# Kernel tuning notes

Measured on AMD Instinct MI355X. Metric: run time of the kernel, lower is better.

## Reference

```python
import jax, jax.numpy as jnp
import numpy as np
import math

N, E, D, H = 50000, 1600000, 128, 8
DH = D // H  # per-head dim
EPS = 1e-5   # batchnorm eps


def _attn(q_in, k_in, v_in, Wq, Wk, Wv, src, dst):
    # GAT-style edge attention: score = exp(clip(<K[src],Q[dst]>/sqrt(DH), -5, 5))
    Q = (q_in @ Wq.T).reshape(-1, H, DH)
    K = (k_in @ Wk.T).reshape(-1, H, DH)
    V = (v_in @ Wv.T).reshape(-1, H, DH)
    score = jnp.exp(jnp.clip((K[src] * Q[dst]).sum(-1) / math.sqrt(DH), -5.0, 5.0))  # [E,H]
    wV = jax.ops.segment_sum(V[src] * score[:, :, None], dst, num_segments=N)  # [N,H,DH]
    z = jax.ops.segment_sum(score, dst, num_segments=N)                         # [N,H]
    return (wV / z[:, :, None]).reshape(-1, D)


def _bn(x, gamma, beta):
    # BatchNorm1d in training mode: biased batch stats over nodes
    m = x.mean(0)
    v = x.var(0)
    return (x - m) / jnp.sqrt(v + EPS) * gamma + beta


def setup_inputs() -> dict:
    key = jax.random.key(0)
    ks = iter(jax.random.split(key, 48))

    def w(shape, scale=None):
        s = scale if scale is not None else 1.0 / math.sqrt(shape[-1])
        return jax.random.normal(next(ks), shape, jnp.float32) * s

    inp = dict(
        h=w((N, D), 1.0),
        sv=w((N, D), 1.0),
        src=jax.random.randint(next(ks), (E,), 0, N, jnp.int32),
        dst=jax.random.randint(next(ks), (E,), 0, N, jnp.int32),
    )
    for nm in ["Wq_sv", "Wk_sv", "Wv_sv", "Wq_cv", "Wk_cv", "Wv_cv",
               "Wq_sh", "Wk_sh", "Wv_sh"]:
        inp[nm] = w((D, D))
    inp.update(
        Wo=w((D, 2 * D)), bo=jnp.zeros((D,), jnp.float32),
        Wo_h=w((D, 2 * D)), bo_h=jnp.zeros((D,), jnp.float32),
        W1=w((2 * D, D)), b1=jnp.zeros((2 * D,), jnp.float32),
        W2=w((D, 2 * D)), b2=jnp.zeros((D,), jnp.float32),
        W1h=w((2 * D, D)), b1h=jnp.zeros((2 * D,), jnp.float32),
        W2h=w((D, 2 * D)), b2h=jnp.zeros((D,), jnp.float32),
        Wg1=w((D, D)), bg1=jnp.zeros((D,), jnp.float32),
        Wg2=w((D, D)), bg2=jnp.zeros((D,), jnp.float32),
        gbn1=jnp.ones((D,), jnp.float32), bbn1=jnp.zeros((D,), jnp.float32),
        gbn2=jnp.ones((D,), jnp.float32), bbn2=jnp.zeros((D,), jnp.float32),
        gbn1h=jnp.ones((D,), jnp.float32), bbn1h=jnp.zeros((D,), jnp.float32),
        gbn2h=jnp.ones((D,), jnp.float32), bbn2h=jnp.zeros((D,), jnp.float32),
    )
    return inp


def reference(h, sv, src, dst,
              Wq_sv, Wk_sv, Wv_sv, Wq_cv, Wk_cv, Wv_cv, Wq_sh, Wk_sh, Wv_sh,
              Wo, bo, Wo_h, bo_h,
              W1, b1, W2, b2, W1h, b1h, W2h, b2h,
              Wg1, bg1, Wg2, bg2,
              gbn1, bbn1, gbn2, bbn2, gbn1h, bbn1h, gbn2h, bbn2h):
    h_in1, sv_in1 = h, sv
    # --- h branch ---
    a_self = _attn(h, h, h, Wq_sv, Wk_sv, Wv_sv, src, dst)
    a_cross = _attn(h, sv, sv, Wq_cv, Wk_cv, Wv_cv, src, dst)
    hO = jnp.concatenate([a_self, a_cross], -1) @ Wo.T + bo
    h1 = _bn(h_in1 + hO, gbn1, bbn1)
    ffn = jax.nn.relu(h1 @ W1.T + b1) @ W2.T + b2
    h_out = _bn(h1 + ffn, gbn2, bbn2)
    # --- state-vector branch ---
    a_self_h = _attn(sv, sv, sv, Wq_sh, Wk_sh, Wv_sh, src, dst)
    # faithful to source: cross_attention_v weights reused here
    a_cross_h = _attn(sv, h_in1, h_in1, Wq_cv, Wk_cv, Wv_cv, src, dst)
    svO = jnp.concatenate([a_self_h, a_cross_h], -1) @ Wo_h.T + bo_h
    g1 = jax.nn.sigmoid(h_in1 @ Wg1.T + bg1)
    sv1 = _bn((1.0 - g1) * sv_in1 + g1 * svO, gbn1h, bbn1h)
    ffn_h = jax.nn.relu(sv1 @ W1h.T + b1h) @ W2h.T + b2h
    g2 = jax.nn.sigmoid(h_in1 @ Wg2.T + bg2)
    sv_out = _bn((1.0 - g2) * sv1 + g2 * ffn_h, gbn2h, bbn2h)
    return (h_out, sv_out)
```

## Files before the change

kernel.cpp:

```cpp
#include <hip/hip_runtime.h>

typedef _Float16 f16x8 __attribute__((ext_vector_type(8)));
typedef _Float16 f16x2 __attribute__((ext_vector_type(2)));
typedef __fp16 fp16x2_raw __attribute__((ext_vector_type(2)));
typedef float f32x4 __attribute__((ext_vector_type(4)));
typedef float f32x2 __attribute__((ext_vector_type(2)));
typedef unsigned int uint32;
typedef unsigned short ushort16;
typedef unsigned char uchar;

#define EPS_BN 1e-5f

__device__ __forceinline__ uint32 pk16(float a, float b){
  fp16x2_raw h = __builtin_amdgcn_cvt_pkrtz(a, b);
  return *(uint32*)&h;
}
__device__ __forceinline__ ushort16 f2h(float f){
  _Float16 h = (_Float16)f;
  union { _Float16 h; ushort16 u; } c; c.h = h; return c.u;
}
__device__ __forceinline__ uchar f2fp8(float f){
  uint32 p = __builtin_amdgcn_cvt_pk_fp8_f32(f, f, 0, false);
  return (uchar)(p & 0xff);
}
__device__ __forceinline__ f32x2 fp8pair_lo(uint32 w){
  return __builtin_amdgcn_cvt_pk_f32_fp8(w, false);
}
__device__ __forceinline__ f32x2 fp8pair_hi(uint32 w){
  return __builtin_amdgcn_cvt_pk_f32_fp8(w, true);
}

struct WEnt { const float* s; const float* s2; ushort16* d; int KD, MD, nfrag; };
struct WConv { WEnt e[16]; };

__global__ __launch_bounds__(256) void conv_w_k(WConv a){
  WEnt t = a.e[blockIdx.y];
  int fid = blockIdx.x * 256 + threadIdx.x;
  if (fid >= t.nfrag) return;
  int lane = fid & 63, sm = fid >> 6;
  int MT = t.MD >> 4;
  int s = sm / MT, m = sm - s * MT;
  int row = m * 16 + (lane & 15);
  int col = s * 32 + (lane >> 4) * 8;
  const float* sp = t.s;
  if (t.s2 && row >= 128){ sp = t.s2; row -= 128; }
  const float* p = sp + (size_t)row * t.KD + col;
  uint4 o;
  o.x = pk16(p[0], p[1]); o.y = pk16(p[2], p[3]);
  o.z = pk16(p[4], p[5]); o.w = pk16(p[6], p[7]);
  *(uint4*)(t.d + (size_t)fid * 8) = o;
}

__global__ __launch_bounds__(256) void conv2_k(const float* __restrict__ a, const float* __restrict__ b,
                                               ushort16* __restrict__ da, ushort16* __restrict__ db, int n){
  const float* s = blockIdx.y ? b : a;
  ushort16* d = blockIdx.y ? db : da;
  int i = (blockIdx.x * 256 + threadIdx.x) * 4;
  if (i >= n) return;
  float4 v = *(const float4*)(s + i);
  uint2 p;
  p.x = pk16(v.x, v.y);
  p.y = pk16(v.z, v.w);
  *(uint2*)(d + i) = p;
}

__global__ void hist_k(const int* __restrict__ dst, int* __restrict__ cnt, int E){
  int i = blockIdx.x * blockDim.x + threadIdx.x;
  int stride = gridDim.x * blockDim.x;
  for (; i < E; i += stride) atomicAdd(&cnt[dst[i]], 1);
}

__global__ __launch_bounds__(256) void scan_part_k(const int* __restrict__ cnt, int* __restrict__ bsum, int N){
  int tid = threadIdx.x, lane = tid & 63, wv = tid >> 6;
  int base = blockIdx.x * 1024 + tid * 4;
  int ts = 0;
  #pragma unroll
  for (int j = 0; j < 4; j++) if (base + j < N) ts += cnt[base + j];
  #pragma unroll
  for (int d = 1; d < 64; d <<= 1) ts += __shfl_xor(ts, d);
  __shared__ int wt[4];
  if (lane == 0) wt[wv] = ts;
  __syncthreads();
  if (tid == 0) bsum[blockIdx.x] = wt[0] + wt[1] + wt[2] + wt[3];
}

__global__ __launch_bounds__(64) void scan_top_k(int* __restrict__ bsum, int nb){
  int tid = threadIdx.x;
  int v = (tid < nb) ? bsum[tid] : 0;
  int inc = v;
  #pragma unroll
  for (int d = 1; d < 64; d <<= 1){
    int t = __shfl_up(inc, d);
    if (tid >= d) inc += t;
  }
  if (tid < nb) bsum[tid] = inc - v;
}

__global__ __launch_bounds__(256) void scan_out_k(const int* __restrict__ cnt, const int* __restrict__ bsum,
                                                  int* __restrict__ row_off, int* __restrict__ cursor,
                                                  int* __restrict__ bcur,
                                                  int N, int E, int shift){
  int tid = threadIdx.x, lane = tid & 63, wv = tid >> 6;
  int base = blockIdx.x * 1024 + tid * 4;
  int c[4]; int ts = 0;
  #pragma unroll
  for (int j = 0; j < 4; j++){ c[j] = (base + j < N) ? cnt[base + j] : 0; ts += c[j]; }
  int inc = ts;
  #pragma unroll
  for (int d = 1; d < 64; d <<= 1){
    int t = __shfl_up(inc, d);
    if (lane >= d) inc += t;
  }
  int wexcl = inc - ts;
  __shared__ int wt[4];
  if (lane == 63) wt[wv] = inc;
  __syncthreads();
  int woff = 0;
  for (int w = 0; w < 4; w++) if (w < wv) woff += wt[w];
  int off = bsum[blockIdx.x] + woff + wexcl;
  int mask = (1 << shift) - 1;
  #pragma unroll
  for (int j = 0; j < 4; j++){
    int d = base + j;
    if (d < N){
      row_off[d] = off; cursor[d] = off;
      if ((d & mask) == 0) bcur[d >> shift] = off;
      off += c[j];
    }
  }
  if (blockIdx.x == 0 && tid == 0) row_off[N] = E;
}

#define BIN_TB 512
#define BIN_TILE 4096
__global__ __launch_bounds__(512) void bin_k(const int* __restrict__ src, const int* __restrict__ dst,
                                             int* __restrict__ bcur, uint2* __restrict__ ebuf,
                                             int E, int shift, int B){
  __shared__ int lhist[128];
  __shared__ int lstart[128];
  __shared__ int gbase[128];
  __shared__ uint2 lpair[BIN_TILE];
  int tid = threadIdx.x;
  int base = blockIdx.x * BIN_TILE;
  int cnt = E - base; if (cnt > BIN_TILE) cnt = BIN_TILE;
  if (tid < 128) lhist[tid] = 0;
  __syncthreads();
  int myb[8], myrank[8];
  uint2 myp[8];
  int nmine = 0;
  #pragma unroll
  for (int j = 0; j < 8; j++){
    int i = tid + j * BIN_TB;
    if (i < cnt){
      int s = src[base + i], d = dst[base + i];
      int b = d >> shift;
      myp[nmine] = make_uint2((uint32)s, (uint32)d);
      myb[nmine] = b;
      myrank[nmine] = atomicAdd(&lhist[b], 1);
      nmine++;
    }
  }
  __syncthreads();
  if (tid == 0){
    int run = 0;
    for (int b = 0; b < B; b++){ lstart[b] = run; run += lhist[b]; }
  }
  __syncthreads();
  if (tid < B) gbase[tid] = atomicAdd(&bcur[tid], lhist[tid]);
  for (int j = 0; j < nmine; j++){
    lpair[lstart[myb[j]] + myrank[j]] = myp[j];
  }
  __syncthreads();
  for (int i = tid; i < cnt; i += BIN_TB){
    uint2 p = lpair[i];
    int b = (int)(p.y >> shift);
    ebuf[gbase[b] + (i - lstart[b])] = p;
  }
}

__global__ __launch_bounds__(512) void bfill_k(const uint2* __restrict__ ebuf, const int* __restrict__ row_off,
                                               int* __restrict__ cursor, int* __restrict__ esrc,
                                               int shift, int N){
  int b = blockIdx.x;
  int d0 = b << shift;
  int d1 = (b + 1) << shift; if (d1 > N) d1 = N;
  if (d0 >= N) return;
  int e0 = row_off[d0], e1 = row_off[d1];
  for (int i = e0 + (int)threadIdx.x; i < e1; i += 512){
    uint2 p = ebuf[i];
    int pos = atomicAdd(&cursor[p.y], 1);
    esrc[pos] = (int)p.x;
  }
}

__global__ __launch_bounds__(256) void gemm_qkv_k(
    const ushort16* __restrict__ Xq, const ushort16* __restrict__ Xkv,
    const ushort16* __restrict__ Wq, const ushort16* __restrict__ Wk, const ushort16* __restrict__ Wv,
    ushort16* __restrict__ Qo, uchar* __restrict__ KV8, int N)
{
  __shared__ _Float16 Qs[4][16 * 136];
  __shared__ uchar Ks[4][16 * 136];
  __shared__ uchar Vs[4][16 * 136];
  int lane = threadIdx.x & 63, wv = threadIdx.x >> 6;
  int l15 = lane & 15, kq = lane >> 4;
  int rowbase = (blockIdx.x * 4 + wv) * 16;
  int row = rowbase + l15;
  int rc = row < N ? row : N - 1;
  const f16x8* aq = (const f16x8*)(Xq + (size_t)rc * 128 + kq * 8);
  const f16x8* ak = (const f16x8*)(Xkv + (size_t)rc * 128 + kq * 8);
  f16x8 Aq[4], Ak[4];
  #pragma unroll
  for (int s = 0; s < 4; s++){ Aq[s] = aq[s * 4]; Ak[s] = ak[s * 4]; }
  const f16x8* Wqf = (const f16x8*)Wq;
  const f16x8* Wkf = (const f16x8*)Wk;
  const f16x8* Wvf = (const f16x8*)Wv;
  f32x4 q[8], k[8], v[8];
  #pragma unroll
  for (int m = 0; m < 8; m++){ q[m] = (f32x4)(0.f); k[m] = (f32x4)(0.f); v[m] = (f32x4)(0.f); }
  #pragma unroll
  for (int s = 0; s < 4; s++){
    #pragma unroll
    for (int m = 0; m < 8; m++){
      int fi = (s * 8 + m) * 64 + lane;
      q[m] = __builtin_amdgcn_mfma_f32_16x16x32_f16(Aq[s], Wqf[fi], q[m], 0, 0, 0);
      k[m] = __builtin_amdgcn_mfma_f32_16x16x32_f16(Ak[s], Wkf[fi], k[m], 0, 0, 0);
      v[m] = __builtin_amdgcn_mfma_f32_16x16x32_f16(Ak[s], Wvf[fi], v[m], 0, 0, 0);
    }
  }
  #pragma unroll
  for (int m = 0; m < 8; m++){
    int col = m * 16 + l15;
    #pragma unroll
    for (int r = 0; r < 4; r++){
      int lrow = kq * 4 + r;
      Qs[wv][lrow * 136 + col] = (_Float16)q[m][r];
      Ks[wv][lrow * 136 + col] = f2fp8(k[m][r]);
      Vs[wv][lrow * 136 + col] = f2fp8(v[m][r]);
    }
  }
  #pragma unroll
  for (int p = 0; p < 4; p++){
    int lrow = p * 4 + (lane >> 4);
    int rr = rowbase + lrow;
    int col8 = l15 * 8;
    if (rr < N){
      uint4 qv = *(uint4*)&Qs[wv][lrow * 136 + col8];
      *(uint4*)(Qo + (size_t)rr * 128 + col8) = qv;
      uint2 kv = *(uint2*)&Ks[wv][lrow * 136 + col8];
      *(uint2*)(KV8 + (size_t)rr * 256 + col8) = kv;
      uint2 vv = *(uint2*)&Vs[wv][lrow * 136 + col8];
      *(uint2*)(KV8 + (size_t)rr * 256 + 128 + col8) = vv;
    }
  }
}

template<int KD, int MD, int EPI, int ABN, int ST, int GS>
__global__ __launch_bounds__(256) void gemm_k(
    const ushort16* __restrict__ X, const ushort16* __restrict__ W,
    const float* __restrict__ bias, const float* __restrict__ bias2,
    const ushort16* __restrict__ resb, const ushort16* __restrict__ gatep,
    const float* __restrict__ rstats, const float* __restrict__ rg, const float* __restrict__ rb,
    const float* __restrict__ astats, const float* __restrict__ ag, const float* __restrict__ ab,
    ushort16* __restrict__ outb, float* __restrict__ stats_out, int N, float invN)
{
  constexpr int KS = KD / 32;
  constexpr int MT = MD / 16;
  constexpr int LSTR = MD + 8;
  __shared__ _Float16 Os[4][16 * LSTR];
  int lane = threadIdx.x & 63, wv = threadIdx.x >> 6;
  int l15 = lane & 15, kq = lane >> 4;
  int rowbase = (blockIdx.x * 4 + wv) * 16;
  int row = rowbase + l15;
  int rc = row < N ? row : N - 1;
  const f16x8* ap = (const f16x8*)(X + (size_t)rc * KD + kq * 8);
  f16x8 a[KS];
  #pragma unroll
  for (int s = 0; s < KS; s++) a[s] = ap[s * 4];
  if constexpr (ABN){
    #pragma unroll
    for (int s = 0; s < KS; s++){
      #pragma unroll
      for (int j = 0; j < 8; j++){
        int c = s * 32 + kq * 8 + j;
        float mm = astats[c] * invN;
        float var = astats[128 + c] * invN - mm * mm;
        float rs = rsqrtf(var + EPS_BN);
        float scc = rs * ag[c];
        float shh = ab[c] - mm * scc;
        a[s][j] = (_Float16)((float)a[s][j] * scc + shh);
      }
    }
  }
  const f16x8* Wf = (const f16x8*)W;
  f32x4 acc[MT];
  #pragma unroll
  for (int m = 0; m < MT; m++) acc[m] = (f32x4)(0.f);
  #pragma unroll
  for (int s = 0; s < KS; s++){
    #pragma unroll
    for (int m = 0; m < MT; m++){
      acc[m] = __builtin_amdgcn_mfma_f32_16x16x32_f16(a[s], Wf[(s * MT + m) * 64 + lane], acc[m], 0, 0, 0);
    }
  }
  float ps[MT], ps2[MT];
  if constexpr (ST){
    #pragma unroll
    for (int m = 0; m < MT; m++){ ps[m] = 0.f; ps2[m] = 0.f; }
  }
  int r0 = rowbase + kq * 4;
  #pragma unroll
  for (int m = 0; m < MT; m++){
    int col = m * 16 + l15;
    float bv;
    if (bias2 && col >= 128) bv = bias2[col - 128];
    else bv = bias[col];
    float sc = 0.f, sh = 0.f;
    if constexpr (EPI == 5 || EPI == 6){
      float mm = rstats[col] * invN;
      float var = rstats[128 + col] * invN - mm * mm;
      float rs = rsqrtf(var + EPS_BN);
      sc = rs * rg[col]; sh = rb[col] - mm * sc;
    }
    #pragma unroll
    for (int r = 0; r < 4; r++){
      int rr = r0 + r;
      float v;
      {
        int rrc = rr < N ? rr : N - 1;
        v = acc[m][r] + bv;
        if constexpr (EPI == 1) v = fmaxf(v, 0.f);
        if constexpr (EPI == 2) v = 1.f / (1.f + __expf(-v));
        if constexpr (EPI == 3){
          union { ushort16 u; _Float16 h; } cv; cv.u = resb[(size_t)rrc * 128 + col];
          v += (float)cv.h;
        }
        if constexpr (EPI == 5){
          union { ushort16 u; _Float16 h; } cv; cv.u = resb[(size_t)rrc * 128 + col];
          v += (float)cv.h * sc + sh;
        }
        if constexpr (EPI == 4 || EPI == 6){
          union { ushort16 u; _Float16 h; } gv; gv.u = gatep[(size_t)rrc * GS + col];
          union { ushort16 u; _Float16 h; } cv; cv.u = resb[(size_t)rrc * 128 + col];
          float g = (float)gv.h;
          float rv = (float)cv.h;
          if constexpr (EPI == 6) rv = rv * sc + sh;
          v = (1.f - g) * rv + g * v;
        }
      }
      Os[wv][(kq * 4 + r) * LSTR + col] = (_Float16)v;
      if constexpr (ST){
        if (rr < N){ ps[m] += v; ps2[m] += v * v; }
      }
    }
  }
  if constexpr (MD == 128){
    #pragma unroll
    for (int p = 0; p < 4; p++){
      int lrow = p * 4 + (lane >> 4);
      int rr = rowbase + lrow;
      int col8 = l15 * 8;
      if (rr < N){
        uint4 ov = *(uint4*)&Os[wv][lrow * LSTR + col8];
        *(uint4*)(outb + (size_t)rr * MD + col8) = ov;
      }
    }
  } else {
    #pragma unroll
    for (int p = 0; p < 8; p++){
      int lrow = p * 2 + (lane >> 5);
      int rr = rowbase + lrow;
      int col8 = (lane & 31) * 8;
      if (rr < N){
        uint4 ov = *(uint4*)&Os[wv][lrow * LSTR + col8];
        *(uint4*)(outb + (size_t)rr * MD + col8) = ov;
      }
    }
  }
  if constexpr (ST){
    __shared__ float sst[4][128];
    __shared__ float sst2[4][128];
    #pragma unroll
    for (int m = 0; m < MT; m++){
      float s = ps[m], s2 = ps2[m];
      s  += __shfl_xor(s, 16);  s  += __shfl_xor(s, 32);
      s2 += __shfl_xor(s2, 16); s2 += __shfl_xor(s2, 32);
      if (lane < 16){ sst[wv][m * 16 + l15] = s; sst2[wv][m * 16 + l15] = s2; }
    }
    __syncthreads();
    int tid = threadIdx.x;
    if (tid < 128){
      atomicAdd(&stats_out[tid], sst[0][tid] + sst[1][tid] + sst[2][tid] + sst[3][tid]);
    } else {
      int c = tid - 128;
      atomicAdd(&stats_out[tid], sst2[0][c] + sst2[1][c] + sst2[2][c] + sst2[3][c]);
    }
  }
}

__global__ __launch_bounds__(256) void attn4_k(
    const ushort16* __restrict__ Qa, const ushort16* __restrict__ Qb,
    const ushort16* __restrict__ Qc, const ushort16* __restrict__ Qd,
    const uchar* __restrict__ KVa, const uchar* __restrict__ KVb,
    const uchar* __restrict__ KVc, const uchar* __restrict__ KVd,
    const int* __restrict__ row_off, const int* __restrict__ esrc,
    ushort16* __restrict__ cat_h, ushort16* __restrict__ cat_sv, int N)
{
  int wv = threadIdx.x >> 6, lane = threadIdx.x & 63;
  int n = blockIdx.x * 4 + wv;
  if (n >= N) return;
  int h = lane >> 5, j = lane & 31;
  uint32 j4 = (uint32)j * 4u;
  const float QS = 0.25f * 1.44269504088896f;
  const float CL = 7.21347520444482f;
  const ushort16* Qp[4] = {Qa, Qb, Qc, Qd};
  const uchar* KVp[4] = {KVa, KVb, KVc, KVd};
  f32x2 q01[4], q23[4];
  #pragma unroll
  for (int t = 0; t < 4; t++){
    uint2 u = *(const uint2*)(Qp[t] + (size_t)n * 128 + j4);
    f16x2 t0 = *(f16x2*)&u.x, t1 = *(f16x2*)&u.y;
    q01[t].x = (float)t0.x * QS; q01[t].y = (float)t0.y * QS;
    q23[t].x = (float)t1.x * QS; q23[t].y = (float)t1.y * QS;
  }
  int e0 = row_off[n], e1 = row_off[n + 1];
  int itmax = (e1 - e0 + 1) >> 1;
  f32x2 ac01[4], ac23[4];
  #pragma unroll
  for (int t = 0; t < 4; t++){ ac01[t] = (f32x2)(0.f); ac23[t] = (f32x2)(0.f); }
  f32x2 z01 = (f32x2)(0.f), z23 = (f32x2)(0.f);
  int e = e0 + h;
  int s = (e < e1) ? esrc[e] : -1;
  uint32 off = ((uint32)(s < 0 ? 0 : s) << 8) + j4;
  uint32 kc_[4], vc_[4];
  #pragma unroll
  for (int t = 0; t < 4; t++){
    kc_[t] = *(const uint32*)(KVp[t] + off);
    vc_[t] = *(const uint32*)(KVp[t] + off + 128);
  }
  for (int it = 0; it < itmax; ++it){
    int e2 = e + 2;
    int s2 = (e2 < e1) ? esrc[e2] : -1;
    uint32 off2 = ((uint32)(s2 < 0 ? 0 : s2) << 8) + j4;
    uint32 kn_[4], vn_[4];
    #pragma unroll
    for (int t = 0; t < 4; t++){
      kn_[t] = *(const uint32*)(KVp[t] + off2);
      vn_[t] = *(const uint32*)(KVp[t] + off2 + 128);
    }
    if (s >= 0){
      float d[4];
      #pragma unroll
      for (int t = 0; t < 4; t++){
        f32x2 k01 = fp8pair_lo(kc_[t]), k23 = fp8pair_hi(kc_[t]);
        f32x2 dd = k01 * q01[t] + k23 * q23[t];
        d[t] = dd.x + dd.y;
      }
      #pragma unroll
      for (int t = 0; t < 4; t++){
        d[t] += __shfl_xor(d[t], 1);
        d[t] += __shfl_xor(d[t], 2);
      }
      float sc4[4];
      #pragma unroll
      for (int t = 0; t < 4; t++)
        sc4[t] = __builtin_amdgcn_exp2f(__builtin_amdgcn_fmed3f(d[t], -CL, CL));
      #pragma unroll
      for (int t = 0; t < 4; t++){
        f32x2 v01 = fp8pair_lo(vc_[t]), v23 = fp8pair_hi(vc_[t]);
        f32x2 sv; sv.x = sc4[t]; sv.y = sc4[t];
        ac01[t] += sv * v01;
        ac23[t] += sv * v23;
      }
      z01.x += sc4[0]; z01.y += sc4[1];
      z23.x += sc4[2]; z23.y += sc4[3];
    }
    e = e2; s = s2;
    #pragma unroll
    for (int t = 0; t < 4; t++){ kc_[t] = kn_[t]; vc_[t] = vn_[t]; }
  }
  #pragma unroll
  for (int t = 0; t < 4; t++){
    f32x2 x;
    x.x = __shfl_xor(ac01[t].x, 32); x.y = __shfl_xor(ac01[t].y, 32); ac01[t] += x;
    x.x = __shfl_xor(ac23[t].x, 32); x.y = __shfl_xor(ac23[t].y, 32); ac23[t] += x;
  }
  {
    f32x2 x;
    x.x = __shfl_xor(z01.x, 32); x.y = __shfl_xor(z01.y, 32); z01 += x;
    x.x = __shfl_xor(z23.x, 32); x.y = __shfl_xor(z23.y, 32); z23 += x;
  }
  size_t nbh = (size_t)n * 256 + j4;
  uint2 o;
  if (h == 0){
    float rz = __builtin_amdgcn_rcpf(z01.x);
    o.x = pk16(ac01[0].x * rz, ac01[0].y * rz);
    o.y = pk16(ac23[0].x * rz, ac23[0].y * rz);
    *(uint2*)(cat_h + nbh) = o;
    rz = __builtin_amdgcn_rcpf(z23.x);
    o.x = pk16(ac01[2].x * rz, ac01[2].y * rz);
    o.y = pk16(ac23[2].x * rz, ac23[2].y * rz);
    *(uint2*)(cat_sv + nbh) = o;
  } else {
    float rz = __builtin_amdgcn_rcpf(z01.y);
    o.x = pk16(ac01[1].x * rz, ac01[1].y * rz);
    o.y = pk16(ac23[1].x * rz, ac23[1].y * rz);
    *(uint2*)(cat_h + nbh + 128) = o;
    rz = __builtin_amdgcn_rcpf(z23.y);
    o.x = pk16(ac01[3].x * rz, ac01[3].y * rz);
    o.y = pk16(ac23[3].x * rz, ac23[3].y * rz);
    *(uint2*)(cat_sv + nbh + 128) = o;
  }
}

__global__ __launch_bounds__(256) void bn_apply_k(
    const ushort16* __restrict__ x, const float* __restrict__ stats,
    const float* __restrict__ gamma, const float* __restrict__ beta,
    float* __restrict__ outf, int total4, float invN)
{
  int i = blockIdx.x * 256 + threadIdx.x;
  if (i >= total4) return;
  uint2 xp = *(const uint2*)(x + (size_t)i * 4);
  f16x2 x01 = *(f16x2*)&xp.x, x23 = *(f16x2*)&xp.y;
  float xv[4] = {(float)x01.x, (float)x01.y, (float)x23.x, (float)x23.y};
  int c0 = (i * 4) & 127;
  float o[4];
  #pragma unroll
  for (int j = 0; j < 4; j++){
    int c = c0 + j;
    float m = stats[c] * invN;
    float var = stats[128 + c] * invN - m * m;
    float rstd = rsqrtf(var + EPS_BN);
    o[j] = (xv[j] - m) * rstd * gamma[c] + beta[c];
  }
  *(float4*)(outf + (size_t)i * 4) = make_float4(o[0], o[1], o[2], o[3]);
}

extern "C" void kernel_launch(void* const* d_in, const int* in_sizes, int n_in,
                              void* d_out, int out_size, void* d_ws, size_t ws_size,
                              hipStream_t stream) {
  const float* h   = (const float*)d_in[0];
  const float* sv  = (const float*)d_in[1];
  const int* src   = (const int*)d_in[2];
  const int* dst   = (const int*)d_in[3];
  const int N = in_sizes[0] / 128;
  const int E = in_sizes[2];

  char* wsb = (char*)d_ws;
  size_t o = 0;
  auto take = [&](size_t bytes)->size_t{
    size_t r = o;
    o = (o + bytes + 255) & ~(size_t)255;
    return r;
  };
  size_t ebuf_bytes = (size_t)E * 8;
  if (ebuf_bytes < (size_t)N * 256) ebuf_bytes = (size_t)N * 256;
  size_t cnt_off    = take((size_t)N * 4);
  size_t stats_off  = take(4 * 256 * 4);
  size_t rowoff_off = take((size_t)(N + 1) * 4);
  size_t cursor_off = take((size_t)N * 4);
  size_t bsum_off   = take(256 * 4);
  size_t bcur_off   = take(128 * 4);
  size_t esrc_off   = take((size_t)E * 4);
  size_t ebuf_off   = take(ebuf_bytes);
  size_t wpool_off  = take((size_t)376832 * 2);
  size_t hf_off     = take((size_t)N * 128 * 2);
  size_t svf_off    = take((size_t)N * 128 * 2);
  size_t cath_off   = take((size_t)N * 256 * 2);
  size_t catsv_off  = take((size_t)N * 256 * 2);
  size_t K81_off    = take((size_t)N * 128);
  size_t V81_off    = take((size_t)N * 128);
  size_t K82_off    = take((size_t)N * 128);
  size_t V82_off    = take((size_t)N * 128);
  size_t Q1_off     = take((size_t)N * 128 * 2);
  size_t Q2_off     = take((size_t)N * 128 * 2);
  size_t X1_off     = take((size_t)N * 128 * 2);
  size_t X2_off     = take((size_t)N * 128 * 2);
  size_t G_off      = take((size_t)N * 256 * 2);

  int*    cnt     = (int*)(wsb + cnt_off);
  float*  stats   = (float*)(wsb + stats_off);
  int*    row_off = (int*)(wsb + rowoff_off);
  int*    cursor  = (int*)(wsb + cursor_off);
  int*    bsum    = (int*)(wsb + bsum_off);
  int*    bcur    = (int*)(wsb + bcur_off);
  int*    esrc    = (int*)(wsb + esrc_off);
  uint2*  ebuf    = (uint2*)(wsb + ebuf_off);
  ushort16* wpool = (ushort16*)(wsb + wpool_off);
  ushort16* h_f   = (ushort16*)(wsb + hf_off);
  ushort16* sv_f  = (ushort16*)(wsb + svf_off);
  ushort16* cat_h = (ushort16*)(wsb + cath_off);
  ushort16* cat_sv= (ushort16*)(wsb + catsv_off);
  ushort16* Q1    = (ushort16*)(wsb + Q1_off);
  ushort16* Q2    = (ushort16*)(wsb + Q2_off);
  ushort16* Xb1   = (ushort16*)(wsb + X1_off);
  ushort16* Xb2   = (ushort16*)(wsb + X2_off);
  ushort16* Gb16  = (ushort16*)(wsb + G_off);
  (void)V81_off; (void)V82_off;

  uchar* KV1 = (uchar*)(wsb + K81_off);
  uchar* KV2 = (uchar*)(wsb + K82_off);
  uchar* KV3 = (uchar*)(wsb + ebuf_off);
  uchar* KV4 = (uchar*)(wsb + G_off);
  ushort16* Q3 = Xb1;
  ushort16* Q4 = Xb2;

  ushort16* Wq_sv = wpool + 0 * 16384;
  ushort16* Wk_sv = wpool + 1 * 16384;
  ushort16* Wv_sv = wpool + 2 * 16384;
  ushort16* Wq_cv = wpool + 3 * 16384;
  ushort16* Wk_cv = wpool + 4 * 16384;
  ushort16* Wv_cv = wpool + 5 * 16384;
  ushort16* Wq_sh = wpool + 6 * 16384;
  ushort16* Wk_sh = wpool + 7 * 16384;
  ushort16* Wv_sh = wpool + 8 * 16384;
  ushort16* Wgb   = wpool + 147456;
  ushort16* Wob   = wpool + 180224;
  ushort16* Wohb  = wpool + 212992;
  ushort16* W1b   = wpool + 245760;
  ushort16* W2b   = wpool + 278528;
  ushort16* W1hb  = wpool + 311296;
  ushort16* W2hb  = wpool + 344064;

  const float* bo   = (const float*)d_in[14];
  const float* bo_h = (const float*)d_in[16];
  const float* b1   = (const float*)d_in[18];
  const float* b2   = (const float*)d_in[20];
  const float* b1h  = (const float*)d_in[22];
  const float* b2h  = (const float*)d_in[24];
  const float* bg1  = (const float*)d_in[26];
  const float* bg2  = (const float*)d_in[28];
  const float* gbn1  = (const float*)d_in[29];
  const float* bbn1  = (const float*)d_in[30];
  const float* gbn2  = (const float*)d_in[31];
  const float* bbn2  = (const float*)d_in[32];
  const float* gbn1h = (const float*)d_in[33];
  const float* bbn1h = (const float*)d_in[34];
  const float* gbn2h = (const float*)d_in[35];
  const float* bbn2h = (const float*)d_in[36];

  float* out_h  = (float*)d_out;
  float* out_sv = out_h + (size_t)N * 128;

  (void)hipMemsetAsync(wsb, 0, stats_off + 4 * 256 * 4, stream);

  WConv wc;
  {
    auto set = [&](int i, int din, int din2, size_t dstoff, int KD, int MD){
      wc.e[i].s  = (const float*)d_in[din];
      wc.e[i].s2 = (din2 >= 0) ? (const float*)d_in[din2] : nullptr;
      wc.e[i].d  = wpool + dstoff;
      wc.e[i].KD = KD; wc.e[i].MD = MD;
      wc.e[i].nfrag = KD * MD / 8;
    };
    for (int i = 0; i < 9; i++) set(i, 4 + i, -1, (size_t)i * 16384, 128, 128);
    set(9,  25, 27, 147456, 128, 256);
    set(10, 13, -1, 180224, 256, 128);
    set(11, 15, -1, 212992, 256, 128);
    set(12, 17, -1, 245760, 128, 256);
    set(13, 19, -1, 278528, 256, 128);
    set(14, 21, -1, 311296, 128, 256);
    set(15, 23, -1, 344064, 256, 128);
  }
  conv_w_k<<<dim3(16, 16), 256, 0, stream>>>(wc);

  int nelem = N * 128;
  conv2_k<<<dim3((nelem / 4 + 255) / 256, 2), 256, 0, stream>>>(h, sv, h_f, sv_f, nelem);

  int shift = 9;
  while ((((N - 1) >> shift) + 1) > 128) shift++;
  const int B = ((N - 1) >> shift) + 1;

  const int NB = (N + 1023) / 1024;
  hist_k<<<2048, 256, 0, stream>>>(dst, cnt, E);
  scan_part_k<<<NB, 256, 0, stream>>>(cnt, bsum, N);
  scan_top_k<<<1, 64, 0, stream>>>(bsum, NB);
  scan_out_k<<<NB, 256, 0, stream>>>(cnt, bsum, row_off, cursor, bcur, N, E, shift);
  bin_k<<<(E + BIN_TILE - 1) / BIN_TILE, BIN_TB, 0, stream>>>(src, dst, bcur, ebuf, E, shift, B);
  bfill_k<<<B, 512, 0, stream>>>(ebuf, row_off, cursor, esrc, shift, N);

  const int GB = (N + 63) / 64;
  const int AB = (N + 3) / 4;
  const int T4 = nelem / 4;
  const int APB = (T4 + 255) / 256;
  const float invN = 1.f / (float)N;

  gemm_qkv_k<<<GB, 256, 0, stream>>>(h_f, h_f, Wq_sv, Wk_sv, Wv_sv, Q1, KV1, N);
  gemm_qkv_k<<<GB, 256, 0, stream>>>(h_f, sv_f, Wq_cv, Wk_cv, Wv_cv, Q2, KV2, N);
  gemm_qkv_k<<<GB, 256, 0, stream>>>(sv_f, sv_f, Wq_sh, Wk_sh, Wv_sh, Q3, KV3, N);
  gemm_qkv_k<<<GB, 256, 0, stream>>>(sv_f, h_f, Wq_cv, Wk_cv, Wv_cv, Q4, KV4, N);
  attn4_k<<<AB, 256, 0, stream>>>(Q1, Q2, Q3, Q4, KV1, KV2, KV3, KV4,
                                  row_off, esrc, cat_h, cat_sv, N);

  gemm_k<256,128,3,0,1,256><<<GB, 256, 0, stream>>>(cat_h, Wob, bo, nullptr, h_f, nullptr,
      nullptr, nullptr, nullptr, nullptr, nullptr, nullptr, Xb1, stats, N, invN);
  gemm_k<128,256,1,1,0,256><<<GB, 256, 0, stream>>>(Xb1, W1b, b1, nullptr, nullptr, nullptr,
      nullptr, nullptr, nullptr, stats, gbn1, bbn1, cat_h, nullptr, N, invN);
  gemm_k<256,128,5,0,1,256><<<GB, 256, 0, stream>>>(cat_h, W2b, b2, nullptr, Xb1, nullptr,
      stats, gbn1, bbn1, nullptr, nullptr, nullptr, Xb2, stats + 256, N, invN);
  bn_apply_k<<<APB, 256, 0, stream>>>(Xb2, stats + 256, gbn2, bbn2, out_h, T4, invN);

  gemm_k<128,256,2,0,0,256><<<GB, 256, 0, stream>>>(h_f, Wgb, bg1, bg2, nullptr, nullptr,
      nullptr, nullptr, nullptr, nullptr, nullptr, nullptr, Gb16, nullptr, N, invN);
  gemm_k<256,128,4,0,1,256><<<GB, 256, 0, stream>>>(cat_sv, Wohb, bo_h, nullptr, sv_f, Gb16,
      nullptr, nullptr, nullptr, nullptr, nullptr, nullptr, Xb1, stats + 512, N, invN);
  gemm_k<128,256,1,1,0,256><<<GB, 256, 0, stream>>>(Xb1, W1hb, b1h, nullptr, nullptr, nullptr,
      nullptr, nullptr, nullptr, stats + 512, gbn1h, bbn1h, cat_sv, nullptr, N, invN);
  gemm_k<256,128,6,0,1,256><<<GB, 256, 0, stream>>>(cat_sv, W2hb, b2h, nullptr, Xb1, Gb16 + 128,
      stats + 512, gbn1h, bbn1h, nullptr, nullptr, nullptr, Xb2, stats + 768, N, invN);
  bn_apply_k<<<APB, 256, 0, stream>>>(Xb2, stats + 768, gbn2h, bbn2h, out_sv, T4, invN);
}
```

Measured before the change: 874.7 us.

## Interleave four attention K/V fp8 buffers per node and process four edges per wave

The four K/V fp8 tables are packed into one interleaved 1KB-per-node buffer, so every gathered source node pulls one contiguous 1KB row instead of four scattered 256B rows. The attention kernel now splits each wave into four 16-lane groups, each handling one edge with 8-byte loads per head pair, so four edges are in flight per iteration rather than two. The aim is better gather locality and more memory-level parallelism in the edge loop. In exchange there are more cross-lane reductions at the end, more registers for the accumulators, and the shared big buffer now also aliases the gate buffer, which the later gate GEMM overwrites after attention has finished.

```diff
diff --git a/kernel.cpp b/kernel.cpp
--- a/kernel.cpp
+++ b/kernel.cpp
@@ -14,10 +14,6 @@
 __device__ __forceinline__ uint32 pk16(float a, float b){
   fp16x2_raw h = __builtin_amdgcn_cvt_pkrtz(a, b);
   return *(uint32*)&h;
-}
-__device__ __forceinline__ ushort16 f2h(float f){
-  _Float16 h = (_Float16)f;
-  union { _Float16 h; ushort16 u; } c; c.h = h; return c.u;
 }
 __device__ __forceinline__ uchar f2fp8(float f){
   uint32 p = __builtin_amdgcn_cvt_pk_fp8_f32(f, f, 0, false);
@@ -196,7 +192,7 @@
 __global__ __launch_bounds__(256) void gemm_qkv_k(
     const ushort16* __restrict__ Xq, const ushort16* __restrict__ Xkv,
     const ushort16* __restrict__ Wq, const ushort16* __restrict__ Wk, const ushort16* __restrict__ Wv,
-    ushort16* __restrict__ Qo, uchar* __restrict__ KV8, int N)
+    ushort16* __restrict__ Qo, uchar* __restrict__ KV8, int toff, int N)
 {
   __shared__ _Float16 Qs[4][16 * 136];
   __shared__ uchar Ks[4][16 * 136];
@@ -247,9 +243,9 @@
       uint4 qv = *(uint4*)&Qs[wv][lrow * 136 + col8];
       *(uint4*)(Qo + (size_t)rr * 128 + col8) = qv;
       uint2 kv = *(uint2*)&Ks[wv][lrow * 136 + col8];
-      *(uint2*)(KV8 + (size_t)rr * 256 + col8) = kv;
+      *(uint2*)(KV8 + (size_t)rr * 1024 + toff + col8) = kv;
       uint2 vv = *(uint2*)&Vs[wv][lrow * 136 + col8];
-      *(uint2*)(KV8 + (size_t)rr * 256 + 128 + col8) = vv;
+      *(uint2*)(KV8 + (size_t)rr * 1024 + toff + 128 + col8) = vv;
     }
   }
 }
@@ -400,115 +396,103 @@
 __global__ __launch_bounds__(256) void attn4_k(
     const ushort16* __restrict__ Qa, const ushort16* __restrict__ Qb,
     const ushort16* __restrict__ Qc, const ushort16* __restrict__ Qd,
-    const uchar* __restrict__ KVa, const uchar* __restrict__ KVb,
-    const uchar* __restrict__ KVc, const uchar* __restrict__ KVd,
+    const uchar* __restrict__ KV,
     const int* __restrict__ row_off, const int* __restrict__ esrc,
     ushort16* __restrict__ cat_h, ushort16* __restrict__ cat_sv, int N)
 {
   int wv = threadIdx.x >> 6, lane = threadIdx.x & 63;
   int n = blockIdx.x * 4 + wv;
   if (n >= N) return;
-  int h = lane >> 5, j = lane & 31;
-  uint32 j4 = (uint32)j * 4u;
+  int g = lane >> 4, j = lane & 15;
+  uint32 j8 = (uint32)j * 8u;
   const float QS = 0.25f * 1.44269504088896f;
   const float CL = 7.21347520444482f;
   const ushort16* Qp[4] = {Qa, Qb, Qc, Qd};
-  const uchar* KVp[4] = {KVa, KVb, KVc, KVd};
-  f32x2 q01[4], q23[4];
+  f32x2 q[4][4];
   #pragma unroll
   for (int t = 0; t < 4; t++){
-    uint2 u = *(const uint2*)(Qp[t] + (size_t)n * 128 + j4);
-    f16x2 t0 = *(f16x2*)&u.x, t1 = *(f16x2*)&u.y;
-    q01[t].x = (float)t0.x * QS; q01[t].y = (float)t0.y * QS;
-    q23[t].x = (float)t1.x * QS; q23[t].y = (float)t1.y * QS;
+    uint4 u = *(const uint4*)(Qp[t] + (size_t)n * 128 + j8);
+    f16x2 h0 = *(f16x2*)&u.x, h1 = *(f16x2*)&u.y;
+    f16x2 h2 = *(f16x2*)&u.z, h3 = *(f16x2*)&u.w;
+    q[t][0].x = (float)h0.x * QS; q[t][0].y = (float)h0.y * QS;
+    q[t][1].x = (float)h1.x * QS; q[t][1].y = (float)h1.y * QS;
+    q[t][2].x = (float)h2.x * QS; q[t][2].y = (float)h2.y * QS;
+    q[t][3].x = (float)h3.x * QS; q[t][3].y = (float)h3.y * QS;
   }
   int e0 = row_off[n], e1 = row_off[n + 1];
-  int itmax = (e1 - e0 + 1) >> 1;
-  f32x2 ac01[4], ac23[4];
-  #pragma unroll
-  for (int t = 0; t < 4; t++){ ac01[t] = (f32x2)(0.f); ac23[t] = (f32x2)(0.f); }
-  f32x2 z01 = (f32x2)(0.f), z23 = (f32x2)(0.f);
-  int e = e0 + h;
+  int itmax = (e1 - e0 + 3) >> 2;
+  f32x2 ac[4][4];
+  #pragma unroll
+  for (int t = 0; t < 4; t++){
+    #pragma unroll
+    for (int r = 0; r < 4; r++) ac[t][r] = (f32x2)(0.f);
+  }
+  float z[4] = {0.f, 0.f, 0.f, 0.f};
+  int e = e0 + g;
   int s = (e < e1) ? esrc[e] : -1;
-  uint32 off = ((uint32)(s < 0 ? 0 : s) << 8) + j4;
-  uint32 kc_[4], vc_[4];
+  uint32 off = ((uint32)(s < 0 ? 0 : s) << 10) + j8;
+  uint2 kc[4], vc[4];
   #pragma unroll
   for (int t = 0; t < 4; t++){
-    kc_[t] = *(const uint32*)(KVp[t] + off);
-    vc_[t] = *(const uint32*)(KVp[t] + off + 128);
+    kc[t] = *(const uint2*)(KV + off + t * 256);
+    vc[t] = *(const uint2*)(KV + off + t * 256 + 128);
   }
   for (int it = 0; it < itmax; ++it){
-    int e2 = e + 2;
+    int e2 = e + 4;
     int s2 = (e2 < e1) ? esrc[e2] : -1;
-    uint32 off2 = ((uint32)(s2 < 0 ? 0 : s2) << 8) + j4;
-    uint32 kn_[4], vn_[4];
+    uint32 off2 = ((uint32)(s2 < 0 ? 0 : s2) << 10) + j8;
+    uint2 kn[4], vn[4];
     #pragma unroll
     for (int t = 0; t < 4; t++){
-      kn_[t] = *(const uint32*)(KVp[t] + off2);
-      vn_[t] = *(const uint32*)(KVp[t] + off2 + 128);
+      kn[t] = *(const uint2*)(KV + off2 + t * 256);
+      vn[t] = *(const uint2*)(KV + off2 + t * 256 + 128);
     }
     if (s >= 0){
-      float d[4];
       #pragma unroll
       for (int t = 0; t < 4; t++){
-        f32x2 k01 = fp8pair_lo(kc_[t]), k23 = fp8pair_hi(kc_[t]);
-        f32x2 dd = k01 * q01[t] + k23 * q23[t];
-        d[t] = dd.x + dd.y;
+        f32x2 k0 = fp8pair_lo(kc[t].x), k1 = fp8pair_hi(kc[t].x);
+        f32x2 k2 = fp8pair_lo(kc[t].y), k3 = fp8pair_hi(kc[t].y);
+        f32x2 dd = k0 * q[t][0] + k1 * q[t][1] + k2 * q[t][2] + k3 * q[t][3];
+        float d = dd.x + dd.y;
+        d += __shfl_xor(d, 1);
+        float sc = __builtin_amdgcn_exp2f(__builtin_amdgcn_fmed3f(d, -CL, CL));
+        f32x2 v0 = fp8pair_lo(vc[t].x), v1 = fp8pair_hi(vc[t].x);
+        f32x2 v2 = fp8pair_lo(vc[t].y), v3 = fp8pair_hi(vc[t].y);
+        f32x2 sv; sv.x = sc; sv.y = sc;
+        ac[t][0] += sv * v0; ac[t][1] += sv * v1;
+        ac[t][2] += sv * v2; ac[t][3] += sv * v3;
+        z[t] += sc;
       }
-      #pragma unroll
-      for (int t = 0; t < 4; t++){
-        d[t] += __shfl_xor(d[t], 1);
-        d[t] += __shfl_xor(d[t], 2);
-      }
-      float sc4[4];
-      #pragma unroll
-      for (int t = 0; t < 4; t++)
-        sc4[t] = __builtin_amdgcn_exp2f(__builtin_amdgcn_fmed3f(d[t], -CL, CL));
-      #pragma unroll
-      for (int t = 0; t < 4; t++){
-        f32x2 v01 = fp8pair_lo(vc_[t]), v23 = fp8pair_hi(vc_[t]);
-        f32x2 sv; sv.x = sc4[t]; sv.y = sc4[t];
-        ac01[t] += sv * v01;
-        ac23[t] += sv * v23;
-      }
-      z01.x += sc4[0]; z01.y += sc4[1];
-      z23.x += sc4[2]; z23.y += sc4[3];
-    }
-    e = e2; s = s2;
-    #pragma unroll
-    for (int t = 0; t < 4; t++){ kc_[t] = kn_[t]; vc_[t] = vn_[t]; }
+    }
+    e = e2; s = s2; off = off2;
+    #pragma unroll
+    for (int t = 0; t < 4; t++){ kc[t] = kn[t]; vc[t] = vn[t]; }
   }
   #pragma unroll
   for (int t = 0; t < 4; t++){
-    f32x2 x;
-    x.x = __shfl_xor(ac01[t].x, 32); x.y = __shfl_xor(ac01[t].y, 32); ac01[t] += x;
-    x.x = __shfl_xor(ac23[t].x, 32); x.y = __shfl_xor(ac23[t].y, 32); ac23[t] += x;
-  }
-  {
-    f32x2 x;
-    x.x = __shfl_xor(z01.x, 32); x.y = __shfl_xor(z01.y, 32); z01 += x;
-    x.x = __shfl_xor(z23.x, 32); x.y = __shfl_xor(z23.y, 32); z23 += x;
-  }
-  size_t nbh = (size_t)n * 256 + j4;
-  uint2 o;
-  if (h == 0){
-    float rz = __builtin_amdgcn_rcpf(z01.x);
-    o.x = pk16(ac01[0].x * rz, ac01[0].y * rz);
-    o.y = pk16(ac23[0].x * rz, ac23[0].y * rz);
-    *(uint2*)(cat_h + nbh) = o;
-    rz = __builtin_amdgcn_rcpf(z23.x);
-    o.x = pk16(ac01[2].x * rz, ac01[2].y * rz);
-    o.y = pk16(ac23[2].x * rz, ac23[2].y * rz);
-    *(uint2*)(cat_sv + nbh) = o;
-  } else {
-    float rz = __builtin_amdgcn_rcpf(z01.y);
-    o.x = pk16(ac01[1].x * rz, ac01[1].y * rz);
-    o.y = pk16(ac23[1].x * rz, ac23[1].y * rz);
-    *(uint2*)(cat_h + nbh + 128) = o;
-    rz = __builtin_amdgcn_rcpf(z23.y);
-    o.x = pk16(ac01[3].x * rz, ac01[3].y * rz);
-    o.y = pk16(ac23[3].x * rz, ac23[3].y * rz);
-    *(uint2*)(cat_sv + nbh + 128) = o;
+    #pragma unroll
+    for (int r = 0; r < 4; r++){
+      ac[t][r].x += __shfl_xor(ac[t][r].x, 16);
+      ac[t][r].y += __shfl_xor(ac[t][r].y, 16);
+      ac[t][r].x += __shfl_xor(ac[t][r].x, 32);
+      ac[t][r].y += __shfl_xor(ac[t][r].y, 32);
+    }
+    z[t] += __shfl_xor(z[t], 16);
+    z[t] += __shfl_xor(z[t], 32);
+  }
+  if (g == 0){
+    size_t base = (size_t)n * 256 + j8;
+    #pragma unroll
+    for (int t = 0; t < 4; t++){
+      float rz = __builtin_amdgcn_rcpf(z[t]);
+      uint4 o;
+      o.x = pk16(ac[t][0].x * rz, ac[t][0].y * rz);
+      o.y = pk16(ac[t][1].x * rz, ac[t][1].y * rz);
+      o.z = pk16(ac[t][2].x * rz, ac[t][2].y * rz);
+      o.w = pk16(ac[t][3].x * rz, ac[t][3].y * rz);
+      ushort16* dp = (t < 2) ? cat_h : cat_sv;
+      *(uint4*)(dp + base + (t & 1) * 128) = o;
+    }
   }
 }
 
@@ -552,8 +536,8 @@
     o = (o + bytes + 255) & ~(size_t)255;
     return r;
   };
-  size_t ebuf_bytes = (size_t)E * 8;
-  if (ebuf_bytes < (size_t)N * 256) ebuf_bytes = (size_t)N * 256;
+  size_t big = (size_t)E * 8;
+  if (big < (size_t)N * 1024) big = (size_t)N * 1024;
   size_t cnt_off    = take((size_t)N * 4);
   size_t stats_off  = take(4 * 256 * 4);
   size_t rowoff_off = take((size_t)(N + 1) * 4);
@@ -561,21 +545,16 @@
   size_t bsum_off   = take(256 * 4);
   size_t bcur_off   = take(128 * 4);
   size_t esrc_off   = take((size_t)E * 4);
-  size_t ebuf_off   = take(ebuf_bytes);
+  size_t big_off    = take(big);
   size_t wpool_off  = take((size_t)376832 * 2);
   size_t hf_off     = take((size_t)N * 128 * 2);
   size_t svf_off    = take((size_t)N * 128 * 2);
   size_t cath_off   = take((size_t)N * 256 * 2);
   size_t catsv_off  = take((size_t)N * 256 * 2);
-  size_t K81_off    = take((size_t)N * 128);
-  size_t V81_off    = take((size_t)N * 128);
-  size_t K82_off    = take((size_t)N * 128);
-  size_t V82_off    = take((size_t)N * 128);
   size_t Q1_off     = take((size_t)N * 128 * 2);
   size_t Q2_off     = take((size_t)N * 128 * 2);
   size_t X1_off     = take((size_t)N * 128 * 2);
   size_t X2_off     = take((size_t)N * 128 * 2);
-  size_t G_off      = take((size_t)N * 256 * 2);
 
   int*    cnt     = (int*)(wsb + cnt_off);
   float*  stats   = (float*)(wsb + stats_off);
@@ -584,7 +563,9 @@
   int*    bsum    = (int*)(wsb + bsum_off);
   int*    bcur    = (int*)(wsb + bcur_off);
   int*    esrc    = (int*)(wsb + esrc_off);
-  uint2*  ebuf    = (uint2*)(wsb + ebuf_off);
+  uint2*  ebuf    = (uint2*)(wsb + big_off);
+  uchar*  KVall   = (uchar*)(wsb + big_off);
+  ushort16* Gb16  = (ushort16*)(wsb + big_off);
   ushort16* wpool = (ushort16*)(wsb + wpool_off);
   ushort16* h_f   = (ushort16*)(wsb + hf_off);
   ushort16* sv_f  = (ushort16*)(wsb + svf_off);
@@ -594,13 +575,6 @@
   ushort16* Q2    = (ushort16*)(wsb + Q2_off);
   ushort16* Xb1   = (ushort16*)(wsb + X1_off);
   ushort16* Xb2   = (ushort16*)(wsb + X2_off);
-  ushort16* Gb16  = (ushort16*)(wsb + G_off);
-  (void)V81_off; (void)V82_off;
-
-  uchar* KV1 = (uchar*)(wsb + K81_off);
-  uchar* KV2 = (uchar*)(wsb + K82_off);
-  uchar* KV3 = (uchar*)(wsb + ebuf_off);
-  uchar* KV4 = (uchar*)(wsb + G_off);
   ushort16* Q3 = Xb1;
   ushort16* Q4 = Xb2;
 
@@ -684,12 +658,11 @@
   const int APB = (T4 + 255) / 256;
   const float invN = 1.f / (float)N;
 
-  gemm_qkv_k<<<GB, 256, 0, stream>>>(h_f, h_f, Wq_sv, Wk_sv, Wv_sv, Q1, KV1, N);
-  gemm_qkv_k<<<GB, 256, 0, stream>>>(h_f, sv_f, Wq_cv, Wk_cv, Wv_cv, Q2, KV2, N);
-  gemm_qkv_k<<<GB, 256, 0, stream>>>(sv_f, sv_f, Wq_sh, Wk_sh, Wv_sh, Q3, KV3, N);
-  gemm_qkv_k<<<GB, 256, 0, stream>>>(sv_f, h_f, Wq_cv, Wk_cv, Wv_cv, Q4, KV4, N);
-  attn4_k<<<AB, 256, 0, stream>>>(Q1, Q2, Q3, Q4, KV1, KV2, KV3, KV4,
-                                  row_off, esrc, cat_h, cat_sv, N);
+  gemm_qkv_k<<<GB, 256, 0, stream>>>(h_f, h_f, Wq_sv, Wk_sv, Wv_sv, Q1, KVall, 0, N);
+  gemm_qkv_k<<<GB, 256, 0, stream>>>(h_f, sv_f, Wq_cv, Wk_cv, Wv_cv, Q2, KVall, 256, N);
+  gemm_qkv_k<<<GB, 256, 0, stream>>>(sv_f, sv_f, Wq_sh, Wk_sh, Wv_sh, Q3, KVall, 512, N);
+  gemm_qkv_k<<<GB, 256, 0, stream>>>(sv_f, h_f, Wq_cv, Wk_cv, Wv_cv, Q4, KVall, 768, N);
+  attn4_k<<<AB, 256, 0, stream>>>(Q1, Q2, Q3, Q4, KVall, row_off, esrc, cat_h, cat_sv, N);
 
   gemm_k<256,128,3,0,1,256><<<GB, 256, 0, stream>>>(cat_h, Wob, bo, nullptr, h_f, nullptr,
       nullptr, nullptr, nullptr, nullptr, nullptr, nullptr, Xb1, stats, N, invN);
```

Result: slower. 906.1 us (+3.6%).
